# Kernel optimization log

Hardware: AMD Instinct MI355X
Metric: run time of the kernel (lower is better)

The kernel has to match this reference:

```python
import jax, jax.numpy as jnp
import numpy as np

B, S, D = 4, 2048, 512
H, DK, DV = 8, 64, 64


def setup_inputs() -> dict:
    key = jax.random.key(0)
    ks = jax.random.split(key, 12)
    inv = 1.0 / np.sqrt(D)
    return {
        "query": jax.random.normal(ks[0], (B, S, D), dtype=jnp.float32),
        "value": jax.random.normal(ks[1], (B, S, D), dtype=jnp.float32),
        "attention_mask": jax.random.randint(ks[2], (B, S), 0, 2, dtype=jnp.int32),
        "Wq": jax.random.normal(ks[3], (D, H * DK), dtype=jnp.float32) * inv,
        "bq": jnp.zeros((H * DK,), dtype=jnp.float32),
        "Wk": jax.random.normal(ks[4], (D, H * DK), dtype=jnp.float32) * inv,
        "bk": jnp.zeros((H * DK,), dtype=jnp.float32),
        "Wv": jax.random.normal(ks[5], (D, H * DV), dtype=jnp.float32) * inv,
        "bv": jnp.zeros((H * DV,), dtype=jnp.float32),
        "Wo": jax.random.normal(ks[6], (H * DV, D), dtype=jnp.float32) * inv,
        "bo": jnp.zeros((D,), dtype=jnp.float32),
    }


def _split_heads(x, h):
    b, s, _ = x.shape
    return x.reshape(b, s, h, -1).transpose(0, 2, 1, 3)  # (B,H,S,dh)


def reference(query, value, attention_mask, Wq, bq, Wk, bk, Wv, bv, Wo, bo):
    # QKV projections (activation=None -> identity); key defaults to value
    q = _split_heads(query @ Wq + bq, H)   # (B,H,S,DK)
    k = _split_heads(value @ Wk + bk, H)   # (B,H,S,DK)
    v = _split_heads(value @ Wv + bv, H)   # (B,H,S,DV)

    scores = jnp.einsum("bhqd,bhkd->bhqk", q, k) / jnp.sqrt(jnp.float32(DK))
    # additive mask: m = 1e9*(mask-1), applied on both key and query axes
    m = 1e9 * (attention_mask.astype(jnp.float32) - 1.0)  # (B,S)
    scores = scores + m[:, None, None, :] + m[:, None, :, None]

    weights = jax.nn.softmax(scores, axis=-1)
    ctx = jnp.einsum("bhqk,bhkd->bhqd", weights, v)        # (B,H,S,DV)
    ctx = ctx.transpose(0, 2, 1, 3).reshape(ctx.shape[0], ctx.shape[2], H * DV)
    return ctx @ Wo + bo  # (B,S,D)
```

## Files before the change

kernel.cpp:

```cpp
#include <hip/hip_runtime.h>

#define B_ 4
#define S_ 2048
#define D_ 512
#define H_ 8

typedef __attribute__((ext_vector_type(8))) __bf16 bf16x8;
typedef __attribute__((ext_vector_type(4))) float f32x4;

#define NEGBIG  -1.442695040e9f
#define QSCALE  0.18033688011112042f

__device__ __forceinline__ unsigned pack_rn(float a, float b) {
    union { float f; unsigned u; } ua, ub; ua.f = a; ub.f = b;
    return __builtin_amdgcn_perm(ub.u + 0x8000u, ua.u + 0x8000u, 0x07060302u);
}

__global__ __launch_bounds__(256) void cast_x(
    const float* __restrict__ q, const float* __restrict__ v,
    unsigned short* __restrict__ xq, unsigned short* __restrict__ xv)
{
    const float* src = blockIdx.z ? v : q;
    unsigned short* dst = blockIdx.z ? xv : xq;
    int i = (blockIdx.x * 256 + threadIdx.x) * 8;
    float4 f0 = *(const float4*)&src[i];
    float4 f1 = *(const float4*)&src[i + 4];
    uint4 o;
    o.x = pack_rn(f0.x, f0.y); o.y = pack_rn(f0.z, f0.w);
    o.z = pack_rn(f1.x, f1.y); o.w = pack_rn(f1.z, f1.w);
    *(uint4*)&dst[i] = o;
}

__global__ __launch_bounds__(256) void cast_wt(
    const float* __restrict__ Wq, const float* __restrict__ Wk,
    const float* __restrict__ Wv, const float* __restrict__ Wo,
    unsigned short* __restrict__ Tq, unsigned short* __restrict__ Tk,
    unsigned short* __restrict__ Tv, unsigned short* __restrict__ To)
{
    int z = blockIdx.z;
    const float* W = (z == 0) ? Wq : (z == 1) ? Wk : (z == 2) ? Wv : Wo;
    unsigned short* T = (z == 0) ? Tq : (z == 1) ? Tk : (z == 2) ? Tv : To;
    int n0 = blockIdx.x * 64, k0 = blockIdx.y * 64;
    int tid = threadIdx.x;

    __shared__ float Ts[64][69];
    #pragma unroll
    for (int it = 0; it < 4; it++) {
        int lin = tid + it * 256;
        int kr = lin >> 4, c4 = (lin & 15) * 4;
        float4 v = *(const float4*)&W[(k0 + kr) * 512 + n0 + c4];
        Ts[kr][c4 + 0] = v.x; Ts[kr][c4 + 1] = v.y;
        Ts[kr][c4 + 2] = v.z; Ts[kr][c4 + 3] = v.w;
    }
    __syncthreads();
    int n = tid >> 2, kc = tid & 3;
    unsigned p[8];
    #pragma unroll
    for (int j = 0; j < 8; j++)
        p[j] = pack_rn(Ts[kc * 16 + 2 * j][n], Ts[kc * 16 + 2 * j + 1][n]);
    unsigned short* dst = &T[(n0 + n) * 512 + k0 + kc * 16];
    *(uint4*)dst       = *(uint4*)&p[0];
    *(uint4*)(dst + 8) = *(uint4*)&p[4];
}

__global__ __launch_bounds__(256) void proj_qkv_mfma(
    const unsigned short* __restrict__ Xq, const unsigned short* __restrict__ Xv,
    const unsigned short* __restrict__ Wtq, const unsigned short* __restrict__ Wtk,
    const unsigned short* __restrict__ Wtv,
    const float* __restrict__ bq, const float* __restrict__ bk,
    const float* __restrict__ bv,
    unsigned short* __restrict__ Qb, unsigned short* __restrict__ Kb,
    unsigned short* __restrict__ VtG)
{
    const int z = blockIdx.z;
    const unsigned short* A  = (z == 0) ? Wtq : (z == 1) ? Wtk : Xv;
    const unsigned short* Bm = (z == 0) ? Xq  : (z == 1) ? Xv  : Wtv;
    const float* bias        = (z == 0) ? bq  : (z == 1) ? bk  : bv;
    const int m0 = (z < 2) ? blockIdx.y * 128 : blockIdx.x * 128;
    const int n0 = (z < 2) ? blockIdx.x * 128 : blockIdx.y * 128;

    const int tid = threadIdx.x;
    const int w = tid >> 6, lane = tid & 63;
    const int l15 = lane & 15, quad = lane >> 4;
    const int wm = (w >> 1) * 64, wn = (w & 1) * 64;

    __shared__ unsigned short As[128 * 72];
    __shared__ unsigned short Bs[128 * 72];

    f32x4 acc[4][4];
    #pragma unroll
    for (int i = 0; i < 4; i++)
        #pragma unroll
        for (int j = 0; j < 4; j++) acc[i][j] = (f32x4){0.f, 0.f, 0.f, 0.f};

    for (int k0 = 0; k0 < 512; k0 += 64) {
        __syncthreads();
        #pragma unroll
        for (int it = 0; it < 2; it++) {
            int lin = tid + it * 256;
            int row = lin >> 2, c2 = (lin & 3) * 2;
            *(uint4*)&As[row * 72 + c2 * 8]     = *(const uint4*)&A[(m0 + row) * 512 + k0 + c2 * 8];
            *(uint4*)&As[row * 72 + c2 * 8 + 8] = *(const uint4*)&A[(m0 + row) * 512 + k0 + c2 * 8 + 8];
            *(uint4*)&Bs[row * 72 + c2 * 8]     = *(const uint4*)&Bm[(n0 + row) * 512 + k0 + c2 * 8];
            *(uint4*)&Bs[row * 72 + c2 * 8 + 8] = *(const uint4*)&Bm[(n0 + row) * 512 + k0 + c2 * 8 + 8];
        }
        __syncthreads();
        #pragma unroll
        for (int kc = 0; kc < 2; kc++) {
            bf16x8 a[4], bb[4];
            #pragma unroll
            for (int i = 0; i < 4; i++)
                a[i] = *(const bf16x8*)&As[(wm + 16 * i + l15) * 72 + kc * 32 + quad * 8];
            #pragma unroll
            for (int j = 0; j < 4; j++)
                bb[j] = *(const bf16x8*)&Bs[(wn + 16 * j + l15) * 72 + kc * 32 + quad * 8];
            #pragma unroll
            for (int i = 0; i < 4; i++)
                #pragma unroll
                for (int j = 0; j < 4; j++)
                    acc[i][j] = __builtin_amdgcn_mfma_f32_16x16x32_bf16(a[i], bb[j], acc[i][j], 0, 0, 0);
        }
    }

    if (z == 2) {
        #pragma unroll
        for (int j = 0; j < 4; j++) {
            int N = n0 + wn + 16 * j + l15;
            float bv_ = bias[N];
            int h = N >> 6, d = N & 63;
            #pragma unroll
            for (int i = 0; i < 4; i++) {
                int Mb = m0 + wm + 16 * i + quad * 4;
                int b = Mb >> 11, s = Mb & 2047;
                uint2 o;
                o.x = pack_rn(acc[i][j][0] + bv_, acc[i][j][1] + bv_);
                o.y = pack_rn(acc[i][j][2] + bv_, acc[i][j][3] + bv_);
                *(uint2*)&VtG[((b * H_ + h) * 64 + d) * 2048 + s] = o;
            }
        }
    } else {
        unsigned short* dst = (z == 0) ? Qb : Kb;
        const float scale = (z == 0) ? QSCALE : 1.0f;
        #pragma unroll
        for (int j = 0; j < 4; j++) {
            int sg = n0 + wn + 16 * j + l15;
            int b = sg >> 11, s = sg & 2047;
            #pragma unroll
            for (int i = 0; i < 4; i++) {
                int F = m0 + wm + 16 * i + quad * 4;
                int h = F >> 6, d = F & 63;
                float4 b4 = *(const float4*)&bias[F];
                uint2 o;
                o.x = pack_rn((acc[i][j][0] + b4.x) * scale, (acc[i][j][1] + b4.y) * scale);
                o.y = pack_rn((acc[i][j][2] + b4.z) * scale, (acc[i][j][3] + b4.w) * scale);
                *(uint2*)&dst[((b * H_ + h) * 2048 + s) * 64 + d] = o;
            }
        }
    }
}

__global__ __launch_bounds__(256) void flash_mfma(
    const unsigned short* __restrict__ Qg, const unsigned short* __restrict__ Kg,
    const unsigned short* __restrict__ VtG, const int* __restrict__ amask,
    unsigned short* __restrict__ ctxB)
{
    const int bh = blockIdx.y, b = bh >> 3, h = bh & 7;
    const int q0 = blockIdx.x * 128;
    const int tid = threadIdx.x;
    const int w = tid >> 6, lane = tid & 63;
    const int l15 = lane & 15, quad = lane >> 4;

    __shared__ unsigned short Ks[2][64 * 72];
    __shared__ unsigned short Ps[4][32 * 72];
    __shared__ float Km[4][64];

    const int* amask_b = amask + b * 2048;
    unsigned short* pw = &Ps[w][0];

    bf16x8 qf[2][2];
    float mq[2];
    #pragma unroll
    for (int qb = 0; qb < 2; qb++) {
        int qrow = q0 + w * 32 + qb * 16 + l15;
        const unsigned short* p = &Qg[(bh * 2048 + qrow) * 64 + quad * 8];
        qf[qb][0] = *(const bf16x8*)p;
        qf[qb][1] = *(const bf16x8*)(p + 32);
        mq[qb] = amask_b[qrow] ? 0.f : NEGBIG;
    }

    const int srow = tid >> 2;
    const int sch  = (tid & 3) * 2;
    const unsigned short* kgb = Kg + (long)bh * 2048 * 64;

    {
        uint4 k0a = *(const uint4*)&kgb[srow * 64 + sch * 8];
        uint4 k0b = *(const uint4*)&kgb[srow * 64 + sch * 8 + 8];
        *(uint4*)&Ks[0][srow * 72 + sch * 8]     = k0a;
        *(uint4*)&Ks[0][srow * 72 + sch * 8 + 8] = k0b;
    }
    int mreg = amask_b[lane];

    f32x4 accO[2][4];
    #pragma unroll
    for (int qb = 0; qb < 2; qb++)
        #pragma unroll
        for (int dt = 0; dt < 4; dt++) accO[qb][dt] = (f32x4){0.f, 0.f, 0.f, 0.f};
    float mi[2] = {-3.0e38f, -3.0e38f};
    float li[2] = {0.f, 0.f};

    __syncthreads();

    for (int t = 0; t < 32; t++) {
        const int kt = t * 64;
        const int ktn = (t < 31) ? kt + 64 : kt;
        const int cur = t & 1, nxt = cur ^ 1;

        bf16x8 vf[4][2];
        #pragma unroll
        for (int dt = 0; dt < 4; dt++)
            #pragma unroll
            for (int kc = 0; kc < 2; kc++)
                vf[dt][kc] = *(const bf16x8*)&VtG[(bh * 64 + dt * 16 + l15) * 2048 + kt + kc * 32 + quad * 8];
        uint4 kst0 = *(const uint4*)&kgb[(ktn + srow) * 64 + sch * 8];
        uint4 kst1 = *(const uint4*)&kgb[(ktn + srow) * 64 + sch * 8 + 8];
        Km[w][lane] = mreg ? 0.f : NEGBIG;
        mreg = amask_b[ktn + lane];

        f32x4 kmf[4];
        #pragma unroll
        for (int nt = 0; nt < 4; nt++)
            kmf[nt] = *(const f32x4*)&Km[w][nt * 16 + quad * 4];

        bf16x8 kf[4][2];
        #pragma unroll
        for (int nt = 0; nt < 4; nt++)
            #pragma unroll
            for (int kc = 0; kc < 2; kc++)
                kf[nt][kc] = *(const bf16x8*)&Ks[cur][(nt * 16 + l15) * 72 + kc * 32 + quad * 8];
        f32x4 sc[2][4];
        #pragma unroll
        for (int qb = 0; qb < 2; qb++)
            #pragma unroll
            for (int nt = 0; nt < 4; nt++) {
                sc[qb][nt] = kmf[nt] + mq[qb];
                #pragma unroll
                for (int kc = 0; kc < 2; kc++)
                    sc[qb][nt] = __builtin_amdgcn_mfma_f32_16x16x32_bf16(
                        kf[nt][kc], qf[qb][kc], sc[qb][nt], 0, 0, 0);
            }

        #pragma unroll
        for (int qb = 0; qb < 2; qb++) {
            float mloc = sc[qb][0][0];
            #pragma unroll
            for (int nt = 0; nt < 4; nt++)
                #pragma unroll
                for (int r = 0; r < 4; r++)
                    mloc = fmaxf(mloc, sc[qb][nt][r]);
            mloc = fmaxf(mloc, __shfl_xor(mloc, 16));
            mloc = fmaxf(mloc, __shfl_xor(mloc, 32));
            float mn = fmaxf(mi[qb], mloc);
            float alpha = __builtin_amdgcn_exp2f(mi[qb] - mn);
            float ps = 0.f;
            #pragma unroll
            for (int nt = 0; nt < 4; nt++) {
                float p0 = __builtin_amdgcn_exp2f(sc[qb][nt][0] - mn);
                float p1 = __builtin_amdgcn_exp2f(sc[qb][nt][1] - mn);
                float p2 = __builtin_amdgcn_exp2f(sc[qb][nt][2] - mn);
                float p3 = __builtin_amdgcn_exp2f(sc[qb][nt][3] - mn);
                ps += (p0 + p1) + (p2 + p3);
                int prow = (qb * 16 + l15) * 72 + nt * 16 + quad * 4;
                *(unsigned*)&pw[prow]     = pack_rn(p0, p1);
                *(unsigned*)&pw[prow + 2] = pack_rn(p2, p3);
            }
            ps += __shfl_xor(ps, 16);
            ps += __shfl_xor(ps, 32);
            li[qb] = li[qb] * alpha + ps;
            mi[qb] = mn;
            #pragma unroll
            for (int dt = 0; dt < 4; dt++) {
                accO[qb][dt][0] *= alpha; accO[qb][dt][1] *= alpha;
                accO[qb][dt][2] *= alpha; accO[qb][dt][3] *= alpha;
            }
        }

        #pragma unroll
        for (int qb = 0; qb < 2; qb++) {
            bf16x8 pf0 = *(const bf16x8*)&pw[(qb * 16 + l15) * 72 + quad * 8];
            bf16x8 pf1 = *(const bf16x8*)&pw[(qb * 16 + l15) * 72 + 32 + quad * 8];
            #pragma unroll
            for (int dt = 0; dt < 4; dt++) {
                accO[qb][dt] = __builtin_amdgcn_mfma_f32_16x16x32_bf16(
                    vf[dt][0], pf0, accO[qb][dt], 0, 0, 0);
                accO[qb][dt] = __builtin_amdgcn_mfma_f32_16x16x32_bf16(
                    vf[dt][1], pf1, accO[qb][dt], 0, 0, 0);
            }
        }

        *(uint4*)&Ks[nxt][srow * 72 + sch * 8]     = kst0;
        *(uint4*)&Ks[nxt][srow * 72 + sch * 8 + 8] = kst1;
        __syncthreads();
    }

    #pragma unroll
    for (int qb = 0; qb < 2; qb++) {
        float inv = 1.f / li[qb];
        int q = q0 + w * 32 + qb * 16 + l15;
        int obase = (b * 2048 + q) * 512 + h * 64 + quad * 4;
        #pragma unroll
        for (int dt = 0; dt < 4; dt++) {
            uint2 o;
            o.x = pack_rn(accO[qb][dt][0] * inv, accO[qb][dt][1] * inv);
            o.y = pack_rn(accO[qb][dt][2] * inv, accO[qb][dt][3] * inv);
            *(uint2*)&ctxB[obase + dt * 16] = o;
        }
    }
}

__global__ __launch_bounds__(256) void proj_out_mfma(
    const unsigned short* __restrict__ ctxB, const unsigned short* __restrict__ Wto,
    const float* __restrict__ bo, float* __restrict__ out)
{
    const int m0 = blockIdx.y * 128, n0 = blockIdx.x * 128;
    const int tid = threadIdx.x;
    const int w = tid >> 6, lane = tid & 63;
    const int l15 = lane & 15, quad = lane >> 4;
    const int wm = (w >> 1) * 64, wn = (w & 1) * 64;

    __shared__ unsigned short As[128 * 72];
    __shared__ unsigned short Bs[128 * 72];

    f32x4 acc[4][4];
    #pragma unroll
    for (int i = 0; i < 4; i++)
        #pragma unroll
        for (int j = 0; j < 4; j++) acc[i][j] = (f32x4){0.f, 0.f, 0.f, 0.f};

    for (int k0 = 0; k0 < 512; k0 += 64) {
        __syncthreads();
        #pragma unroll
        for (int it = 0; it < 2; it++) {
            int lin = tid + it * 256;
            int row = lin >> 2, c2 = (lin & 3) * 2;
            *(uint4*)&As[row * 72 + c2 * 8]     = *(const uint4*)&Wto[(m0 + row) * 512 + k0 + c2 * 8];
            *(uint4*)&As[row * 72 + c2 * 8 + 8] = *(const uint4*)&Wto[(m0 + row) * 512 + k0 + c2 * 8 + 8];
            *(uint4*)&Bs[row * 72 + c2 * 8]     = *(const uint4*)&ctxB[(n0 + row) * 512 + k0 + c2 * 8];
            *(uint4*)&Bs[row * 72 + c2 * 8 + 8] = *(const uint4*)&ctxB[(n0 + row) * 512 + k0 + c2 * 8 + 8];
        }
        __syncthreads();
        #pragma unroll
        for (int kc = 0; kc < 2; kc++) {
            bf16x8 a[4], bb[4];
            #pragma unroll
            for (int i = 0; i < 4; i++)
                a[i] = *(const bf16x8*)&As[(wm + 16 * i + l15) * 72 + kc * 32 + quad * 8];
            #pragma unroll
            for (int j = 0; j < 4; j++)
                bb[j] = *(const bf16x8*)&Bs[(wn + 16 * j + l15) * 72 + kc * 32 + quad * 8];
            #pragma unroll
            for (int i = 0; i < 4; i++)
                #pragma unroll
                for (int j = 0; j < 4; j++)
                    acc[i][j] = __builtin_amdgcn_mfma_f32_16x16x32_bf16(a[i], bb[j], acc[i][j], 0, 0, 0);
        }
    }

    #pragma unroll
    for (int j = 0; j < 4; j++) {
        int sg = n0 + wn + 16 * j + l15;
        #pragma unroll
        for (int i = 0; i < 4; i++) {
            int F = m0 + wm + 16 * i + quad * 4;
            float4 b4 = *(const float4*)&bo[F];
            float4 vv;
            vv.x = acc[i][j][0] + b4.x;
            vv.y = acc[i][j][1] + b4.y;
            vv.z = acc[i][j][2] + b4.z;
            vv.w = acc[i][j][3] + b4.w;
            *(float4*)&out[sg * 512 + F] = vv;
        }
    }
}

extern "C" void kernel_launch(void* const* d_in, const int* in_sizes, int n_in,
                              void* d_out, int out_size, void* d_ws, size_t ws_size,
                              hipStream_t stream)
{
    const float* query = (const float*)d_in[0];
    const float* value = (const float*)d_in[1];
    const int*   amask = (const int*)d_in[2];
    const float* Wq = (const float*)d_in[3];
    const float* bq = (const float*)d_in[4];
    const float* Wk = (const float*)d_in[5];
    const float* bk = (const float*)d_in[6];
    const float* Wv = (const float*)d_in[7];
    const float* bv = (const float*)d_in[8];
    const float* Wo = (const float*)d_in[9];
    const float* bo = (const float*)d_in[10];
    float* out = (float*)d_out;

    char* ws = (char*)d_ws;
    const size_t MB = 1 << 20;
    unsigned short* Xbq = (unsigned short*)(ws);
    unsigned short* Xbv = (unsigned short*)(ws + 8 * MB);
    unsigned short* Wtq = (unsigned short*)(ws + 16 * MB);
    unsigned short* Wtk = (unsigned short*)(ws + 16 * MB + MB / 2);
    unsigned short* Wtv = (unsigned short*)(ws + 17 * MB);
    unsigned short* Wto = (unsigned short*)(ws + 17 * MB + MB / 2);
    unsigned short* Qb  = (unsigned short*)(ws + 18 * MB);
    unsigned short* Kb  = (unsigned short*)(ws + 26 * MB);
    unsigned short* VtG = (unsigned short*)(ws + 34 * MB);
    unsigned short* ctx = (unsigned short*)(ws + 42 * MB);

    cast_x<<<dim3(2048, 1, 2), 256, 0, stream>>>(query, value, Xbq, Xbv);
    cast_wt<<<dim3(8, 8, 4), 256, 0, stream>>>(Wq, Wk, Wv, Wo, Wtq, Wtk, Wtv, Wto);
    proj_qkv_mfma<<<dim3(64, 4, 3), 256, 0, stream>>>(Xbq, Xbv, Wtq, Wtk, Wtv,
                                                      bq, bk, bv, Qb, Kb, VtG);
    flash_mfma<<<dim3(16, 32), 256, 0, stream>>>(Qb, Kb, VtG, amask, ctx);
    proj_out_mfma<<<dim3(64, 4), 256, 0, stream>>>(ctx, Wto, bo, out);
}
```

Before: 213.4 us.

## Stream K tiles directly into registers and skip rescale when max barely grows

The flash attention kernel no longer stages K through shared memory with per-tile barriers. Each wave now loads K fragments and precomputed float mask values straight from global memory into double-buffered registers, using a software pipeline with two steps per iteration. A lazy rescaling rule only updates the running max and rescales the accumulator when some lane's max exceeds the old max by more than 4, and MFMA sections are wrapped in raised wave priority. This removes LDS traffic and syncs at the cost of more global loads per wave (K is no longer shared across the four waves) and higher register pressure. A new small kernel converts the mask to float once and writes it into the workspace, reusing the region that held Xbq.

```diff
diff --git a/kernel.cpp b/kernel.cpp
--- a/kernel.cpp
+++ b/kernel.cpp
@@ -31,6 +31,19 @@
     *(uint4*)&dst[i] = o;
 }
 
+__global__ __launch_bounds__(256) void mask_f(
+    const int* __restrict__ am, float* __restrict__ Mf)
+{
+    int i = (blockIdx.x * 256 + threadIdx.x) * 4;
+    int4 m = *(const int4*)&am[i];
+    float4 o;
+    o.x = m.x ? 0.f : NEGBIG;
+    o.y = m.y ? 0.f : NEGBIG;
+    o.z = m.z ? 0.f : NEGBIG;
+    o.w = m.w ? 0.f : NEGBIG;
+    *(float4*)&Mf[i] = o;
+}
+
 __global__ __launch_bounds__(256) void cast_wt(
     const float* __restrict__ Wq, const float* __restrict__ Wk,
     const float* __restrict__ Wv, const float* __restrict__ Wo,
@@ -159,9 +172,9 @@
     }
 }
 
-__global__ __launch_bounds__(256) void flash_mfma(
+__global__ __launch_bounds__(256, 2) void flash_mfma(
     const unsigned short* __restrict__ Qg, const unsigned short* __restrict__ Kg,
-    const unsigned short* __restrict__ VtG, const int* __restrict__ amask,
+    const unsigned short* __restrict__ VtG, const float* __restrict__ Mf,
     unsigned short* __restrict__ ctxB)
 {
     const int bh = blockIdx.y, b = bh >> 3, h = bh & 7;
@@ -170,12 +183,19 @@
     const int w = tid >> 6, lane = tid & 63;
     const int l15 = lane & 15, quad = lane >> 4;
 
-    __shared__ unsigned short Ks[2][64 * 72];
     __shared__ unsigned short Ps[4][32 * 72];
-    __shared__ float Km[4][64];
-
-    const int* amask_b = amask + b * 2048;
     unsigned short* pw = &Ps[w][0];
+
+    const float* mfb = Mf + b * 2048;
+
+    const unsigned short* kp[4];
+    const unsigned short* vp[4];
+    #pragma unroll
+    for (int i = 0; i < 4; i++) {
+        kp[i] = Kg  + ((long)bh * 2048 + i * 16 + l15) * 64 + quad * 8;
+        vp[i] = VtG + ((long)bh * 64 + i * 16 + l15) * 2048 + quad * 8;
+    }
+    const float* mp = mfb + quad * 4;
 
     bf16x8 qf[2][2];
     float mq[2];
@@ -185,20 +205,8 @@
         const unsigned short* p = &Qg[(bh * 2048 + qrow) * 64 + quad * 8];
         qf[qb][0] = *(const bf16x8*)p;
         qf[qb][1] = *(const bf16x8*)(p + 32);
-        mq[qb] = amask_b[qrow] ? 0.f : NEGBIG;
-    }
-
-    const int srow = tid >> 2;
-    const int sch  = (tid & 3) * 2;
-    const unsigned short* kgb = Kg + (long)bh * 2048 * 64;
-
-    {
-        uint4 k0a = *(const uint4*)&kgb[srow * 64 + sch * 8];
-        uint4 k0b = *(const uint4*)&kgb[srow * 64 + sch * 8 + 8];
-        *(uint4*)&Ks[0][srow * 72 + sch * 8]     = k0a;
-        *(uint4*)&Ks[0][srow * 72 + sch * 8 + 8] = k0b;
-    }
-    int mreg = amask_b[lane];
+        mq[qb] = mfb[qrow];
+    }
 
     f32x4 accO[2][4];
     #pragma unroll
@@ -208,59 +216,74 @@
     float mi[2] = {-3.0e38f, -3.0e38f};
     float li[2] = {0.f, 0.f};
 
-    __syncthreads();
-
-    for (int t = 0; t < 32; t++) {
-        const int kt = t * 64;
-        const int ktn = (t < 31) ? kt + 64 : kt;
-        const int cur = t & 1, nxt = cur ^ 1;
+    bf16x8 kfA[4][2], kfB[4][2];
+    f32x4 kmA[4], kmB[4];
+
+    auto LOADK = [&](bf16x8 (&kf)[4][2], f32x4 (&km)[4], int t) {
+        const int ko = t * 64;
+        #pragma unroll
+        for (int nt = 0; nt < 4; nt++) {
+            kf[nt][0] = *(const bf16x8*)(kp[nt] + ko * 64);
+            kf[nt][1] = *(const bf16x8*)(kp[nt] + ko * 64 + 32);
+            km[nt]    = *(const f32x4*)(mp + ko + nt * 16);
+        }
+    };
+
+    auto STEP = [&](const bf16x8 (&kf)[4][2], const f32x4 (&km)[4], int t) {
+        const int ko = t * 64;
 
         bf16x8 vf[4][2];
         #pragma unroll
-        for (int dt = 0; dt < 4; dt++)
-            #pragma unroll
-            for (int kc = 0; kc < 2; kc++)
-                vf[dt][kc] = *(const bf16x8*)&VtG[(bh * 64 + dt * 16 + l15) * 2048 + kt + kc * 32 + quad * 8];
-        uint4 kst0 = *(const uint4*)&kgb[(ktn + srow) * 64 + sch * 8];
-        uint4 kst1 = *(const uint4*)&kgb[(ktn + srow) * 64 + sch * 8 + 8];
-        Km[w][lane] = mreg ? 0.f : NEGBIG;
-        mreg = amask_b[ktn + lane];
-
-        f32x4 kmf[4];
-        #pragma unroll
-        for (int nt = 0; nt < 4; nt++)
-            kmf[nt] = *(const f32x4*)&Km[w][nt * 16 + quad * 4];
-
-        bf16x8 kf[4][2];
-        #pragma unroll
-        for (int nt = 0; nt < 4; nt++)
-            #pragma unroll
-            for (int kc = 0; kc < 2; kc++)
-                kf[nt][kc] = *(const bf16x8*)&Ks[cur][(nt * 16 + l15) * 72 + kc * 32 + quad * 8];
+        for (int dt = 0; dt < 4; dt++) {
+            vf[dt][0] = *(const bf16x8*)(vp[dt] + ko);
+            vf[dt][1] = *(const bf16x8*)(vp[dt] + ko + 32);
+        }
+
         f32x4 sc[2][4];
         #pragma unroll
         for (int qb = 0; qb < 2; qb++)
             #pragma unroll
             for (int nt = 0; nt < 4; nt++) {
-                sc[qb][nt] = kmf[nt] + mq[qb];
+                f32x4 c = km[nt];
+                c[0] += mq[qb]; c[1] += mq[qb]; c[2] += mq[qb]; c[3] += mq[qb];
+                sc[qb][nt] = c;
+            }
+        __builtin_amdgcn_s_setprio(1);
+        #pragma unroll
+        for (int qb = 0; qb < 2; qb++)
+            #pragma unroll
+            for (int nt = 0; nt < 4; nt++)
                 #pragma unroll
                 for (int kc = 0; kc < 2; kc++)
                     sc[qb][nt] = __builtin_amdgcn_mfma_f32_16x16x32_bf16(
                         kf[nt][kc], qf[qb][kc], sc[qb][nt], 0, 0, 0);
-            }
+        __builtin_amdgcn_s_setprio(0);
 
         #pragma unroll
         for (int qb = 0; qb < 2; qb++) {
-            float mloc = sc[qb][0][0];
-            #pragma unroll
-            for (int nt = 0; nt < 4; nt++)
-                #pragma unroll
-                for (int r = 0; r < 4; r++)
-                    mloc = fmaxf(mloc, sc[qb][nt][r]);
+            float mloc = fmaxf(fmaxf(sc[qb][0][0], sc[qb][0][1]),
+                               fmaxf(sc[qb][0][2], sc[qb][0][3]));
+            #pragma unroll
+            for (int nt = 1; nt < 4; nt++)
+                mloc = fmaxf(mloc, fmaxf(fmaxf(sc[qb][nt][0], sc[qb][nt][1]),
+                                         fmaxf(sc[qb][nt][2], sc[qb][nt][3])));
             mloc = fmaxf(mloc, __shfl_xor(mloc, 16));
             mloc = fmaxf(mloc, __shfl_xor(mloc, 32));
-            float mn = fmaxf(mi[qb], mloc);
-            float alpha = __builtin_amdgcn_exp2f(mi[qb] - mn);
+
+            float mn = mi[qb];
+            if (!__all(mloc <= mn + 4.f)) {
+                float mo = mn;
+                mn = fmaxf(mo, mloc);
+                float alpha = __builtin_amdgcn_exp2f(mo - mn);
+                li[qb] *= alpha;
+                #pragma unroll
+                for (int dt = 0; dt < 4; dt++) {
+                    accO[qb][dt][0] *= alpha; accO[qb][dt][1] *= alpha;
+                    accO[qb][dt][2] *= alpha; accO[qb][dt][3] *= alpha;
+                }
+                mi[qb] = mn;
+            }
+
             float ps = 0.f;
             #pragma unroll
             for (int nt = 0; nt < 4; nt++) {
@@ -275,19 +298,14 @@
             }
             ps += __shfl_xor(ps, 16);
             ps += __shfl_xor(ps, 32);
-            li[qb] = li[qb] * alpha + ps;
-            mi[qb] = mn;
-            #pragma unroll
-            for (int dt = 0; dt < 4; dt++) {
-                accO[qb][dt][0] *= alpha; accO[qb][dt][1] *= alpha;
-                accO[qb][dt][2] *= alpha; accO[qb][dt][3] *= alpha;
-            }
+            li[qb] += ps;
         }
 
         #pragma unroll
         for (int qb = 0; qb < 2; qb++) {
             bf16x8 pf0 = *(const bf16x8*)&pw[(qb * 16 + l15) * 72 + quad * 8];
             bf16x8 pf1 = *(const bf16x8*)&pw[(qb * 16 + l15) * 72 + 32 + quad * 8];
+            __builtin_amdgcn_s_setprio(1);
             #pragma unroll
             for (int dt = 0; dt < 4; dt++) {
                 accO[qb][dt] = __builtin_amdgcn_mfma_f32_16x16x32_bf16(
@@ -295,11 +313,16 @@
                 accO[qb][dt] = __builtin_amdgcn_mfma_f32_16x16x32_bf16(
                     vf[dt][1], pf1, accO[qb][dt], 0, 0, 0);
             }
-        }
-
-        *(uint4*)&Ks[nxt][srow * 72 + sch * 8]     = kst0;
-        *(uint4*)&Ks[nxt][srow * 72 + sch * 8 + 8] = kst1;
-        __syncthreads();
+            __builtin_amdgcn_s_setprio(0);
+        }
+    };
+
+    LOADK(kfA, kmA, 0);
+    for (int t = 0; t < 32; t += 2) {
+        LOADK(kfB, kmB, t + 1);
+        STEP(kfA, kmA, t);
+        LOADK(kfA, kmA, (t + 2 < 32) ? t + 2 : 31);
+        STEP(kfB, kmB, t + 1);
     }
 
     #pragma unroll
@@ -411,11 +434,13 @@
     unsigned short* Kb  = (unsigned short*)(ws + 26 * MB);
     unsigned short* VtG = (unsigned short*)(ws + 34 * MB);
     unsigned short* ctx = (unsigned short*)(ws + 42 * MB);
+    float* Mf = (float*)(ws);
 
     cast_x<<<dim3(2048, 1, 2), 256, 0, stream>>>(query, value, Xbq, Xbv);
     cast_wt<<<dim3(8, 8, 4), 256, 0, stream>>>(Wq, Wk, Wv, Wo, Wtq, Wtk, Wtv, Wto);
     proj_qkv_mfma<<<dim3(64, 4, 3), 256, 0, stream>>>(Xbq, Xbv, Wtq, Wtk, Wtv,
                                                       bq, bk, bv, Qb, Kb, VtG);
-    flash_mfma<<<dim3(16, 32), 256, 0, stream>>>(Qb, Kb, VtG, amask, ctx);
+    mask_f<<<dim3(8), 256, 0, stream>>>(amask, Mf);
+    flash_mfma<<<dim3(16, 32), 256, 0, stream>>>(Qb, Kb, VtG, Mf, ctx);
     proj_out_mfma<<<dim3(64, 4), 256, 0, stream>>>(ctx, Wto, bo, out);
 }
```

Result: slower. 270.1 us (+26.6%).
